# Optimization experiments

Measured on AMD Instinct MI355X. Metric: run time of the kernel, lower is better.

## Reference

```python
import jax, jax.numpy as jnp
import numpy as np

N_NODES = 50000
N_EDGES = 800000
N_RELS = 65
D = 64
N_GRAPHS = 512


def setup_inputs() -> dict:
    key = jax.random.key(0)
    ks = jax.random.split(key, 20)
    inp = {
        "node_feats": jax.random.normal(ks[0], (N_NODES, D), dtype=jnp.float32),
        "etypes": jax.random.randint(ks[1], (N_EDGES,), 0, N_RELS),
        "src": jax.random.randint(ks[2], (N_EDGES,), 0, N_NODES),
        "dst": jax.random.randint(ks[3], (N_EDGES,), 0, N_NODES),
        "graph_ids": jnp.sort(jax.random.randint(ks[4], (N_NODES,), 0, N_GRAPHS)),
    }
    s = 1.0 / np.sqrt(D)
    # 3 RGCN layers: per-relation weights (basis with num_bases=num_rels == full) + bias
    for i, k in zip(range(1, 4), (ks[5], ks[6], ks[7])):
        inp[f"W_rel{i}"] = jax.random.normal(k, (N_RELS, D, D), dtype=jnp.float32) * s
        inp[f"b{i}"] = jnp.zeros((D,), dtype=jnp.float32)
    # 3 FC layers
    for i, k in zip(range(1, 4), (ks[8], ks[9], ks[10])):
        inp[f"fc_W{i}"] = jax.random.normal(k, (D, D), dtype=jnp.float32) * s
        inp[f"fc_b{i}"] = jnp.zeros((D,), dtype=jnp.float32)
    inp["pred_W"] = jax.random.normal(ks[11], (D, 2), dtype=jnp.float32) * s
    inp["pred_b"] = jnp.zeros((2,), dtype=jnp.float32)
    return inp


def _rgcn_layer(h, W, b, etypes, src, dst):
    # all-relation projection: [N, R, K]
    proj = jnp.einsum('nd,rdk->nrk', h, W)
    # per-edge gather of relation-specific message: [E, K]
    msg = proj[src, etypes]
    # scatter-sum into destination nodes
    agg = jax.ops.segment_sum(msg, dst, num_segments=h.shape[0])
    return jax.nn.relu(agg + b)


def reference(node_feats, etypes, src, dst, graph_ids,
              W_rel1, b1, W_rel2, b2, W_rel3, b3,
              fc_W1, fc_b1, fc_W2, fc_b2, fc_W3, fc_b3,
              pred_W, pred_b):
    h = node_feats
    h = _rgcn_layer(h, W_rel1, b1, etypes, src, dst)
    h = _rgcn_layer(h, W_rel2, b2, etypes, src, dst)
    h = _rgcn_layer(h, W_rel3, b3, etypes, src, dst)
    # sum-pool nodes per graph: [G, D]
    g = jax.ops.segment_sum(h, graph_ids, num_segments=N_GRAPHS)
    g = jax.nn.relu(g @ fc_W1 + fc_b1)
    g = jax.nn.relu(g @ fc_W2 + fc_b2)
    g = jax.nn.relu(g @ fc_W3 + fc_b3)
    return g @ pred_W + pred_b
```

## Files before the change

### kernel.cpp

```cpp
#include <hip/hip_runtime.h>
#include <hip/hip_bf16.h>

#define N_NODES 50000
#define N_EDGES 800000
#define N_RELS 65
#define DIM 64
#define N_GRAPHS 512

#define SORT_BLOCKS 256
#define CHUNK ((N_EDGES + SORT_BLOCKS - 1) / SORT_BLOCKS)

#define SCAN_BLK 512
#define NSCAN_BLKS ((N_NODES + SCAN_BLK - 1) / SCAN_BLK)

#define MSG_BLOCKS 1024
#define NWAVES (MSG_BLOCKS * 4)

typedef __attribute__((ext_vector_type(8))) short short8;
typedef __attribute__((ext_vector_type(4))) float f32x4;


__global__ void conv_h_kernel(const float* __restrict__ x, __hip_bfloat16* __restrict__ y) {
    int i = blockIdx.x * 256 + threadIdx.x;
    if (i < N_NODES * DIM) y[i] = __float2bfloat16(x[i]);
}

__global__ void conv_wt3_kernel(const float* __restrict__ W1, const float* __restrict__ W2,
                                const float* __restrict__ W3,
                                __hip_bfloat16* __restrict__ Wt1,
                                __hip_bfloat16* __restrict__ Wt2,
                                __hip_bfloat16* __restrict__ Wt3) {
    const int n = N_RELS * DIM * DIM;
    int i = blockIdx.x * 256 + threadIdx.x;
    if (i >= 3 * n) return;
    int which = i / n, j = i - which * n;
    const float* W = (which == 0) ? W1 : (which == 1) ? W2 : W3;
    __hip_bfloat16* Wt = (which == 0) ? Wt1 : (which == 1) ? Wt2 : Wt3;
    int r = j >> 12, rest = j & 4095;
    int nn = rest >> 6, k = rest & 63;
    Wt[(size_t)r * 4096 + nn * 64 + k] = __float2bfloat16(W[(size_t)r * 4096 + k * 64 + nn]);
}


__global__ __launch_bounds__(256) void hist2_kernel(const int* __restrict__ et,
                                                    int* __restrict__ blk_hist) {
    __shared__ int lh[N_RELS];
    int t = threadIdx.x, b = blockIdx.x;
    if (t < N_RELS) lh[t] = 0;
    __syncthreads();
    int lo = b * CHUNK;
    int hi = lo + CHUNK; if (hi > N_EDGES) hi = N_EDGES;
    for (int i = lo + t; i < hi; i += 256) atomicAdd(&lh[et[i]], 1);
    __syncthreads();
    if (t < N_RELS) blk_hist[b * N_RELS + t] = lh[t];
}

__global__ __launch_bounds__(256) void relwave_kernel(const int* __restrict__ blk_hist,
                                                      int* __restrict__ blk_off,
                                                      int* __restrict__ rel_tot) {
    int wave = blockIdx.x * 4 + (threadIdx.x >> 6);
    int lane = threadIdx.x & 63;
    if (wave >= N_RELS) return;
    int run = 0;
    for (int c = 0; c < SORT_BLOCKS; c += 64) {
        int b = c + lane;
        int v = blk_hist[b * N_RELS + wave];
        int x = v;
        #pragma unroll
        for (int off = 1; off < 64; off <<= 1) {
            int y = __shfl_up(x, off);
            if (lane >= off) x += y;
        }
        blk_off[b * N_RELS + wave] = run + x - v;
        run += __shfl(x, 63);
    }
    if (lane == 0) rel_tot[wave] = run;
}

__global__ __launch_bounds__(128) void relbase_kernel(const int* __restrict__ rel_tot,
                                                      int* __restrict__ rel_ptr,
                                                      int* __restrict__ tile_base) {
    __shared__ int tot[N_RELS];
    int t = threadIdx.x;
    if (t < N_RELS) tot[t] = rel_tot[t];
    __syncthreads();
    if (t == 0) {
        int s = 0, tt = 0;
        for (int q = 0; q < N_RELS; ++q) {
            rel_ptr[q] = s; s += tot[q];
            tile_base[q] = tt; tt += (tot[q] + 15) >> 4;
        }
        rel_ptr[N_RELS] = N_EDGES;
        tile_base[N_RELS] = tt;
    }
}

__global__ __launch_bounds__(256) void scatter2_kernel(
    const int* __restrict__ et, const int* __restrict__ src,
    const int* __restrict__ dst, const int* __restrict__ blk_off,
    const int* __restrict__ rel_ptr,
    int* __restrict__ src_s, int* __restrict__ dst_s) {
    __shared__ int cur[N_RELS];
    int t = threadIdx.x, b = blockIdx.x;
    if (t < N_RELS) cur[t] = blk_off[b * N_RELS + t] + rel_ptr[t];
    __syncthreads();
    int lo = b * CHUNK;
    int hi = lo + CHUNK; if (hi > N_EDGES) hi = N_EDGES;
    for (int i = lo + t; i < hi; i += 256) {
        int r = et[i];
        int p = atomicAdd(&cur[r], 1);
        src_s[p] = src[i];
        dst_s[p] = dst[i];
    }
}


__global__ void histdst_kernel(const int* __restrict__ dst, int* __restrict__ cnt_d) {
    int i = blockIdx.x * 256 + threadIdx.x;
    if (i < N_EDGES) atomicAdd(&cnt_d[dst[i]], 1);
}

__global__ __launch_bounds__(SCAN_BLK) void scanblk_kernel(const int* __restrict__ cnt,
                                                           int* __restrict__ outv,
                                                           int* __restrict__ blk_tot) {
    __shared__ int tmp[SCAN_BLK];
    int t = threadIdx.x;
    int i = blockIdx.x * SCAN_BLK + t;
    int v = (i < N_NODES) ? cnt[i] : 0;
    tmp[t] = v;
    __syncthreads();
    for (int off = 1; off < SCAN_BLK; off <<= 1) {
        int add = (t >= off) ? tmp[t - off] : 0;
        __syncthreads();
        tmp[t] += add;
        __syncthreads();
    }
    if (i < N_NODES) outv[i] = tmp[t] - v;
    if (t == SCAN_BLK - 1) blk_tot[blockIdx.x] = tmp[t];
}

__global__ void scantop_kernel(int* __restrict__ blk_tot, int* __restrict__ blk_base) {
    if (threadIdx.x == 0 && blockIdx.x == 0) {
        int run = 0;
        for (int b = 0; b < NSCAN_BLKS; ++b) { blk_base[b] = run; run += blk_tot[b]; }
    }
}

__global__ __launch_bounds__(SCAN_BLK) void scanadd_kernel(int* __restrict__ outv,
                                                           const int* __restrict__ blk_base) {
    int i = blockIdx.x * SCAN_BLK + threadIdx.x;
    if (i < N_NODES) outv[i] += blk_base[blockIdx.x];
}

__global__ void dpos_kernel(const int* __restrict__ dst_s, int* __restrict__ cursor,
                            int* __restrict__ dpos) {
    int i = blockIdx.x * 256 + threadIdx.x;
    if (i < N_EDGES) dpos[i] = atomicAdd(&cursor[dst_s[i]], 1);
}


__global__ void histgid_kernel(const int* __restrict__ gid, int* __restrict__ cnt_g) {
    int i = blockIdx.x * 256 + threadIdx.x;
    if (i < N_NODES) atomicAdd(&cnt_g[gid[i]], 1);
}

__global__ __launch_bounds__(512) void scangid_kernel(const int* __restrict__ cnt_g,
                                                      int* __restrict__ g_ptr) {
    __shared__ int tmp[512];
    int t = threadIdx.x;
    int v = (t < N_GRAPHS) ? cnt_g[t] : 0;
    tmp[t] = v;
    __syncthreads();
    for (int off = 1; off < 512; off <<= 1) {
        int add = (t >= off) ? tmp[t - off] : 0;
        __syncthreads();
        tmp[t] += add;
        __syncthreads();
    }
    if (t < N_GRAPHS) g_ptr[t] = tmp[t] - v;
}


__global__ __launch_bounds__(256) void msg_mfma_kernel(
    const __hip_bfloat16* __restrict__ hb, const __hip_bfloat16* __restrict__ Wt,
    const int* __restrict__ rel_ptr, const int* __restrict__ tile_base,
    const int* __restrict__ src_s, const int* __restrict__ dpos,
    __hip_bfloat16* __restrict__ msg) {
    __shared__ __align__(16) unsigned short stA[4][16 * 72];
    __shared__ __align__(16) float stC[4][16 * 68];

    int t = threadIdx.x;
    int w = t >> 6, lane = t & 63;
    int quad = lane >> 4, m16 = lane & 15;
    int wave = blockIdx.x * 4 + w;

    int ntiles = tile_base[N_RELS];
    int tpw = (ntiles + NWAVES - 1) / NWAVES;
    int T = wave * tpw;
    int T1 = T + tpw; if (T1 > ntiles) T1 = ntiles;
    if (T >= T1) return;

    unsigned short* sa = &stA[w][0];
    float* sc = &stC[w][0];

    int r = 0;
    while (T >= tile_base[r + 1]) ++r;

    while (T < T1) {
        int chunk_end = tile_base[r + 1]; if (chunk_end > T1) chunk_end = T1;
        int seg_end = rel_ptr[r + 1];

        const __hip_bfloat16* Wr = Wt + (size_t)r * (DIM * DIM);
        short8 bf00 = *(const short8*)(Wr + (0 * 16 + m16) * DIM + 0 * 32 + quad * 8);
        short8 bf01 = *(const short8*)(Wr + (1 * 16 + m16) * DIM + 0 * 32 + quad * 8);
        short8 bf02 = *(const short8*)(Wr + (2 * 16 + m16) * DIM + 0 * 32 + quad * 8);
        short8 bf03 = *(const short8*)(Wr + (3 * 16 + m16) * DIM + 0 * 32 + quad * 8);
        short8 bf10 = *(const short8*)(Wr + (0 * 16 + m16) * DIM + 1 * 32 + quad * 8);
        short8 bf11 = *(const short8*)(Wr + (1 * 16 + m16) * DIM + 1 * 32 + quad * 8);
        short8 bf12 = *(const short8*)(Wr + (2 * 16 + m16) * DIM + 1 * 32 + quad * 8);
        short8 bf13 = *(const short8*)(Wr + (3 * 16 + m16) * DIM + 1 * 32 + quad * 8);

        for (; T < chunk_end; ++T) {
            int e0 = rel_ptr[r] + (T - tile_base[r]) * 16;
            int rows = seg_end - e0; if (rows > 16) rows = 16;

            int sv = 0, dp = 0;
            if (lane < rows) { sv = src_s[e0 + lane]; dp = dpos[e0 + lane]; }

            #pragma unroll
            for (int half = 0; half < 2; ++half) {
                int row = (lane >> 3) + half * 8;
                int s = __shfl(sv, row);
                uint4 d; d.x = 0u; d.y = 0u; d.z = 0u; d.w = 0u;
                if (row < rows)
                    d = *(const uint4*)(hb + (size_t)s * DIM + (lane & 7) * 8);
                *(uint4*)&sa[row * 72 + (lane & 7) * 8] = d;
            }

            short8 a0 = *(const short8*)&sa[m16 * 72 + quad * 8];
            short8 a1 = *(const short8*)&sa[m16 * 72 + 32 + quad * 8];

            f32x4 c0 = {0.f, 0.f, 0.f, 0.f}, c1 = c0, c2 = c0, c3 = c0;
            c0 = __builtin_amdgcn_mfma_f32_16x16x32_bf16(a0, bf00, c0, 0, 0, 0);
            c1 = __builtin_amdgcn_mfma_f32_16x16x32_bf16(a0, bf01, c1, 0, 0, 0);
            c2 = __builtin_amdgcn_mfma_f32_16x16x32_bf16(a0, bf02, c2, 0, 0, 0);
            c3 = __builtin_amdgcn_mfma_f32_16x16x32_bf16(a0, bf03, c3, 0, 0, 0);
            c0 = __builtin_amdgcn_mfma_f32_16x16x32_bf16(a1, bf10, c0, 0, 0, 0);
            c1 = __builtin_amdgcn_mfma_f32_16x16x32_bf16(a1, bf11, c1, 0, 0, 0);
            c2 = __builtin_amdgcn_mfma_f32_16x16x32_bf16(a1, bf12, c2, 0, 0, 0);
            c3 = __builtin_amdgcn_mfma_f32_16x16x32_bf16(a1, bf13, c3, 0, 0, 0);

            #pragma unroll
            for (int reg = 0; reg < 4; ++reg) {
                int rr = (quad * 4 + reg) * 68 + m16;
                sc[rr +  0] = c0[reg];
                sc[rr + 16] = c1[reg];
                sc[rr + 32] = c2[reg];
                sc[rr + 48] = c3[reg];
            }

            int orow = lane >> 2;
            if (orow < rows) {
                int c0i = (lane & 3) * 16;
                float vs[16];
                *(f32x4*)&vs[0]  = *(const f32x4*)&sc[orow * 68 + c0i + 0];
                *(f32x4*)&vs[4]  = *(const f32x4*)&sc[orow * 68 + c0i + 4];
                *(f32x4*)&vs[8]  = *(const f32x4*)&sc[orow * 68 + c0i + 8];
                *(f32x4*)&vs[12] = *(const f32x4*)&sc[orow * 68 + c0i + 12];
                unsigned short us[16];
                #pragma unroll
                for (int i = 0; i < 16; ++i)
                    us[i] = __hip_bfloat16_raw(__float2bfloat16(vs[i])).x;
                int dprow = __shfl(dp, orow);
                __hip_bfloat16* dst = msg + (size_t)dprow * DIM + c0i;
                *(uint4*)dst = *(const uint4*)&us[0];
                *(uint4*)(dst + 8) = *(const uint4*)&us[8];
            }
        }
        ++r;
        while (T < T1 && T >= tile_base[r + 1]) ++r;
    }
}


__global__ __launch_bounds__(256) void agg_kernel(
    const __hip_bfloat16* __restrict__ msg, const int* __restrict__ row_ptr,
    const int* __restrict__ cnt_d, const float* __restrict__ b,
    __hip_bfloat16* __restrict__ hout) {
    int wave = blockIdx.x * 4 + (threadIdx.x >> 6);
    int lane = threadIdx.x & 63;
    if (wave >= N_NODES) return;
    int j0 = row_ptr[wave];
    int n  = cnt_d[wave];
    float a0 = 0.f, a1 = 0.f, a2 = 0.f, a3 = 0.f;
    int j = 0;
    for (; j + 3 < n; j += 4) {
        a0 += __bfloat162float(msg[(size_t)(j0 + j + 0) * DIM + lane]);
        a1 += __bfloat162float(msg[(size_t)(j0 + j + 1) * DIM + lane]);
        a2 += __bfloat162float(msg[(size_t)(j0 + j + 2) * DIM + lane]);
        a3 += __bfloat162float(msg[(size_t)(j0 + j + 3) * DIM + lane]);
    }
    for (; j < n; ++j)
        a0 += __bfloat162float(msg[(size_t)(j0 + j) * DIM + lane]);
    float v = ((a0 + a1) + (a2 + a3)) + b[lane];
    hout[(size_t)wave * DIM + lane] = __float2bfloat16(v > 0.f ? v : 0.f);
}


__global__ __launch_bounds__(256) void pool_seg_kernel(
    const __hip_bfloat16* __restrict__ h, const int* __restrict__ g_ptr,
    const int* __restrict__ cnt_g, float* __restrict__ g) {
    int wave = blockIdx.x * 4 + (threadIdx.x >> 6);
    int lane = threadIdx.x & 63;
    if (wave >= N_GRAPHS) return;
    int j0 = g_ptr[wave];
    int n  = cnt_g[wave];
    float a0 = 0.f, a1 = 0.f;
    int j = 0;
    for (; j + 1 < n; j += 2) {
        a0 += __bfloat162float(h[(size_t)(j0 + j) * DIM + lane]);
        a1 += __bfloat162float(h[(size_t)(j0 + j + 1) * DIM + lane]);
    }
    if (j < n) a0 += __bfloat162float(h[(size_t)(j0 + j) * DIM + lane]);
    g[(size_t)wave * DIM + lane] = a0 + a1;
}


__global__ __launch_bounds__(256) void fc_kernel(
    const float* __restrict__ g,
    const float* __restrict__ W1, const float* __restrict__ b1,
    const float* __restrict__ W2, const float* __restrict__ b2,
    const float* __restrict__ W3, const float* __restrict__ b3,
    const float* __restrict__ pW, const float* __restrict__ pb,
    float* __restrict__ out) {
    int wave = blockIdx.x * 4 + (threadIdx.x >> 6);
    int lane = threadIdx.x & 63;
    if (wave >= N_GRAPHS) return;

    float v = g[(size_t)wave * DIM + lane];

    const float* Ws[3] = {W1, W2, W3};
    const float* bs[3] = {b1, b2, b3};
    for (int l = 0; l < 3; ++l) {
        float acc = bs[l][lane];
        const float* __restrict__ Wl = Ws[l];
        #pragma unroll
        for (int d = 0; d < DIM; ++d)
            acc += __shfl(v, d) * Wl[d * DIM + lane];
        v = acc > 0.f ? acc : 0.f;
    }

    float p0 = v * pW[lane * 2 + 0];
    float p1 = v * pW[lane * 2 + 1];
    #pragma unroll
    for (int off = 32; off > 0; off >>= 1) {
        p0 += __shfl_down(p0, off);
        p1 += __shfl_down(p1, off);
    }
    if (lane == 0) {
        out[wave * 2 + 0] = p0 + pb[0];
        out[wave * 2 + 1] = p1 + pb[1];
    }
}


extern "C" void kernel_launch(void* const* d_in, const int* in_sizes, int n_in,
                              void* d_out, int out_size, void* d_ws, size_t ws_size,
                              hipStream_t stream) {
    const float* node_feats = (const float*)d_in[0];
    const int*   etypes     = (const int*)d_in[1];
    const int*   src        = (const int*)d_in[2];
    const int*   dst        = (const int*)d_in[3];
    const int*   graph_ids  = (const int*)d_in[4];
    const float* W1 = (const float*)d_in[5];
    const float* b1 = (const float*)d_in[6];
    const float* W2 = (const float*)d_in[7];
    const float* b2 = (const float*)d_in[8];
    const float* W3 = (const float*)d_in[9];
    const float* b3 = (const float*)d_in[10];
    const float* fcW1 = (const float*)d_in[11];
    const float* fcb1 = (const float*)d_in[12];
    const float* fcW2 = (const float*)d_in[13];
    const float* fcb2 = (const float*)d_in[14];
    const float* fcW3 = (const float*)d_in[15];
    const float* fcb3 = (const float*)d_in[16];
    const float* pW = (const float*)d_in[17];
    const float* pb = (const float*)d_in[18];
    float* out = (float*)d_out;

    char* p = (char*)d_ws;
    auto alloc = [&](size_t bytes) -> void* {
        void* r = (void*)p;
        p += (bytes + 255) & ~(size_t)255;
        return r;
    };
    int* blk_hist  = (int*)alloc((size_t)SORT_BLOCKS * N_RELS * sizeof(int));
    int* blk_off   = (int*)alloc((size_t)SORT_BLOCKS * N_RELS * sizeof(int));
    int* rel_tot   = (int*)alloc(N_RELS * sizeof(int));
    int* rel_ptr   = (int*)alloc((N_RELS + 1) * sizeof(int));
    int* tile_base = (int*)alloc((N_RELS + 1) * sizeof(int));
    int* src_s     = (int*)alloc((size_t)N_EDGES * sizeof(int));
    int* dst_s     = (int*)alloc((size_t)N_EDGES * sizeof(int));
    int* dpos      = (int*)alloc((size_t)N_EDGES * sizeof(int));
    int* cnt_d     = (int*)alloc((size_t)N_NODES * sizeof(int));
    int* row_ptr   = (int*)alloc((size_t)N_NODES * sizeof(int));
    int* cursor_d  = (int*)alloc((size_t)N_NODES * sizeof(int));
    int* blk_tot   = (int*)alloc(NSCAN_BLKS * sizeof(int));
    int* blk_base  = (int*)alloc(NSCAN_BLKS * sizeof(int));
    int* cnt_g     = (int*)alloc(N_GRAPHS * sizeof(int));
    int* g_ptr     = (int*)alloc(N_GRAPHS * sizeof(int));
    float* g       = (float*)alloc((size_t)N_GRAPHS * DIM * sizeof(float));
    __hip_bfloat16* hb0 = (__hip_bfloat16*)alloc((size_t)N_NODES * DIM * sizeof(__hip_bfloat16));
    __hip_bfloat16* hb1 = (__hip_bfloat16*)alloc((size_t)N_NODES * DIM * sizeof(__hip_bfloat16));
    __hip_bfloat16* Wt1 = (__hip_bfloat16*)alloc((size_t)N_RELS * DIM * DIM * sizeof(__hip_bfloat16));
    __hip_bfloat16* Wt2 = (__hip_bfloat16*)alloc((size_t)N_RELS * DIM * DIM * sizeof(__hip_bfloat16));
    __hip_bfloat16* Wt3 = (__hip_bfloat16*)alloc((size_t)N_RELS * DIM * DIM * sizeof(__hip_bfloat16));
    __hip_bfloat16* msg = (__hip_bfloat16*)alloc((size_t)N_EDGES * DIM * sizeof(__hip_bfloat16));

    const int EBLK = (N_EDGES + 255) / 256;
    const int HBLK = (N_NODES * DIM + 255) / 256;
    const int W3BLK = (3 * N_RELS * DIM * DIM + 255) / 256;
    const int NBLK256 = (N_NODES + 255) / 256;
    const int AGG_BLOCKS = (N_NODES + 3) / 4;

    conv_h_kernel<<<HBLK, 256, 0, stream>>>(node_feats, hb0);
    conv_wt3_kernel<<<W3BLK, 256, 0, stream>>>(W1, W2, W3, Wt1, Wt2, Wt3);

    hist2_kernel<<<SORT_BLOCKS, 256, 0, stream>>>(etypes, blk_hist);
    relwave_kernel<<<(N_RELS + 3) / 4, 256, 0, stream>>>(blk_hist, blk_off, rel_tot);
    relbase_kernel<<<1, 128, 0, stream>>>(rel_tot, rel_ptr, tile_base);
    scatter2_kernel<<<SORT_BLOCKS, 256, 0, stream>>>(etypes, src, dst, blk_off, rel_ptr,
                                                     src_s, dst_s);

    hipMemsetAsync(cnt_d, 0, (size_t)N_NODES * sizeof(int), stream);
    histdst_kernel<<<EBLK, 256, 0, stream>>>(dst, cnt_d);
    scanblk_kernel<<<NSCAN_BLKS, SCAN_BLK, 0, stream>>>(cnt_d, row_ptr, blk_tot);
    scantop_kernel<<<1, 64, 0, stream>>>(blk_tot, blk_base);
    scanadd_kernel<<<NSCAN_BLKS, SCAN_BLK, 0, stream>>>(row_ptr, blk_base);
    hipMemcpyAsync(cursor_d, row_ptr, (size_t)N_NODES * sizeof(int),
                   hipMemcpyDeviceToDevice, stream);
    dpos_kernel<<<EBLK, 256, 0, stream>>>(dst_s, cursor_d, dpos);

    hipMemsetAsync(cnt_g, 0, N_GRAPHS * sizeof(int), stream);
    histgid_kernel<<<NBLK256, 256, 0, stream>>>(graph_ids, cnt_g);
    scangid_kernel<<<1, 512, 0, stream>>>(cnt_g, g_ptr);

    msg_mfma_kernel<<<MSG_BLOCKS, 256, 0, stream>>>(hb0, Wt1, rel_ptr, tile_base,
                                                    src_s, dpos, msg);
    agg_kernel<<<AGG_BLOCKS, 256, 0, stream>>>(msg, row_ptr, cnt_d, b1, hb1);

    msg_mfma_kernel<<<MSG_BLOCKS, 256, 0, stream>>>(hb1, Wt2, rel_ptr, tile_base,
                                                    src_s, dpos, msg);
    agg_kernel<<<AGG_BLOCKS, 256, 0, stream>>>(msg, row_ptr, cnt_d, b2, hb0);

    msg_mfma_kernel<<<MSG_BLOCKS, 256, 0, stream>>>(hb0, Wt3, rel_ptr, tile_base,
                                                    src_s, dpos, msg);
    agg_kernel<<<AGG_BLOCKS, 256, 0, stream>>>(msg, row_ptr, cnt_d, b3, hb1);

    pool_seg_kernel<<<(N_GRAPHS + 3) / 4, 256, 0, stream>>>(hb1, g_ptr, cnt_g, g);
    fc_kernel<<<(N_GRAPHS + 3) / 4, 256, 0, stream>>>(g, fcW1, fcb1, fcW2, fcb2,
                                                      fcW3, fcb3, pW, pb, out);
}
```

Baseline: 452.0 us.

## Prefetch gathers in message kernel, vectorize aggregation, fuse pool+FC and memsets

The message MFMA kernel now software-pipelines its work: it prefetches the next tile's source rows and the index loads two tiles ahead, which is meant to hide gather latency. The aggregation and pooling kernels switch to 16-byte bf16 loads across 8 row groups, followed by a shuffle reduction. Pooling is fused with the FC layers, and the memsets and the cursor memcpy are folded into existing kernels to cut launch count. The trade-off is higher register pressure, and padded tail rows are now loaded with clamped indices instead of zeroed.

```diff
diff --git a/kernel.cpp b/kernel.cpp
--- a/kernel.cpp
+++ b/kernel.cpp
@@ -20,9 +20,12 @@
 typedef __attribute__((ext_vector_type(4))) float f32x4;
 
 
-__global__ void conv_h_kernel(const float* __restrict__ x, __hip_bfloat16* __restrict__ y) {
+__global__ void conv_h_zero_kernel(const float* __restrict__ x, __hip_bfloat16* __restrict__ y,
+                                   int* __restrict__ cnt_d, int* __restrict__ cnt_g) {
     int i = blockIdx.x * 256 + threadIdx.x;
     if (i < N_NODES * DIM) y[i] = __float2bfloat16(x[i]);
+    if (i < N_NODES) cnt_d[i] = 0;
+    if (i < N_GRAPHS) cnt_g[i] = 0;
 }
 
 __global__ void conv_wt3_kernel(const float* __restrict__ W1, const float* __restrict__ W2,
@@ -147,9 +150,14 @@
 }
 
 __global__ __launch_bounds__(SCAN_BLK) void scanadd_kernel(int* __restrict__ outv,
+                                                           int* __restrict__ cursor,
                                                            const int* __restrict__ blk_base) {
     int i = blockIdx.x * SCAN_BLK + threadIdx.x;
-    if (i < N_NODES) outv[i] += blk_base[blockIdx.x];
+    if (i < N_NODES) {
+        int v = outv[i] + blk_base[blockIdx.x];
+        outv[i] = v;
+        cursor[i] = v;
+    }
 }
 
 __global__ void dpos_kernel(const int* __restrict__ dst_s, int* __restrict__ cursor,
@@ -208,6 +216,7 @@
 
     while (T < T1) {
         int chunk_end = tile_base[r + 1]; if (chunk_end > T1) chunk_end = T1;
+        int e_base = rel_ptr[r], t_base = tile_base[r];
         int seg_end = rel_ptr[r + 1];
 
         const __hip_bfloat16* Wr = Wt + (size_t)r * (DIM * DIM);
@@ -220,21 +229,46 @@
         short8 bf12 = *(const short8*)(Wr + (2 * 16 + m16) * DIM + 1 * 32 + quad * 8);
         short8 bf13 = *(const short8*)(Wr + (3 * 16 + m16) * DIM + 1 * 32 + quad * 8);
 
+        auto eidx = [&](int TT) {
+            int i = e_base + (TT - t_base) * 16 + lane;
+            return i < N_EDGES ? i : N_EDGES - 1;
+        };
+
+        int sv_c, dp_c, sv_n = 0, dp_n = 0, sv_nn = 0, dp_nn = 0;
+        uint4 g0_c, g1_c;
+        {
+            int i0 = eidx(T);
+            sv_c = src_s[i0]; dp_c = dpos[i0];
+            int r0 = lane >> 3;
+            int s0 = __shfl(sv_c, r0);
+            int s1 = __shfl(sv_c, r0 + 8);
+            g0_c = *(const uint4*)(hb + (size_t)s0 * DIM + (lane & 7) * 8);
+            g1_c = *(const uint4*)(hb + (size_t)s1 * DIM + (lane & 7) * 8);
+            if (T + 1 < chunk_end) {
+                int i1 = eidx(T + 1);
+                sv_n = src_s[i1]; dp_n = dpos[i1];
+            }
+        }
+
         for (; T < chunk_end; ++T) {
-            int e0 = rel_ptr[r] + (T - tile_base[r]) * 16;
+            int e0 = e_base + (T - t_base) * 16;
             int rows = seg_end - e0; if (rows > 16) rows = 16;
 
-            int sv = 0, dp = 0;
-            if (lane < rows) { sv = src_s[e0 + lane]; dp = dpos[e0 + lane]; }
-
-            #pragma unroll
-            for (int half = 0; half < 2; ++half) {
-                int row = (lane >> 3) + half * 8;
-                int s = __shfl(sv, row);
-                uint4 d; d.x = 0u; d.y = 0u; d.z = 0u; d.w = 0u;
-                if (row < rows)
-                    d = *(const uint4*)(hb + (size_t)s * DIM + (lane & 7) * 8);
-                *(uint4*)&sa[row * 72 + (lane & 7) * 8] = d;
+            int r0 = lane >> 3;
+            *(uint4*)&sa[r0 * 72 + (lane & 7) * 8] = g0_c;
+            *(uint4*)&sa[(r0 + 8) * 72 + (lane & 7) * 8] = g1_c;
+
+            uint4 g0_n, g1_n;
+            bool hasN = (T + 1 < chunk_end);
+            if (hasN) {
+                int s0 = __shfl(sv_n, r0);
+                int s1 = __shfl(sv_n, r0 + 8);
+                g0_n = *(const uint4*)(hb + (size_t)s0 * DIM + (lane & 7) * 8);
+                g1_n = *(const uint4*)(hb + (size_t)s1 * DIM + (lane & 7) * 8);
+            }
+            if (T + 2 < chunk_end) {
+                int i2 = eidx(T + 2);
+                sv_nn = src_s[i2]; dp_nn = dpos[i2];
             }
 
             short8 a0 = *(const short8*)&sa[m16 * 72 + quad * 8];
@@ -271,11 +305,15 @@
                 #pragma unroll
                 for (int i = 0; i < 16; ++i)
                     us[i] = __hip_bfloat16_raw(__float2bfloat16(vs[i])).x;
-                int dprow = __shfl(dp, orow);
+                int dprow = __shfl(dp_c, orow);
                 __hip_bfloat16* dst = msg + (size_t)dprow * DIM + c0i;
                 *(uint4*)dst = *(const uint4*)&us[0];
                 *(uint4*)(dst + 8) = *(const uint4*)&us[8];
             }
+
+            if (hasN) { g0_c = g0_n; g1_c = g1_n; }
+            sv_c = sv_n; dp_c = dp_n;
+            sv_n = sv_nn; dp_n = dp_nn;
         }
         ++r;
         while (T < T1 && T >= tile_base[r + 1]) ++r;
@@ -292,42 +330,44 @@
     if (wave >= N_NODES) return;
     int j0 = row_ptr[wave];
     int n  = cnt_d[wave];
-    float a0 = 0.f, a1 = 0.f, a2 = 0.f, a3 = 0.f;
-    int j = 0;
-    for (; j + 3 < n; j += 4) {
-        a0 += __bfloat162float(msg[(size_t)(j0 + j + 0) * DIM + lane]);
-        a1 += __bfloat162float(msg[(size_t)(j0 + j + 1) * DIM + lane]);
-        a2 += __bfloat162float(msg[(size_t)(j0 + j + 2) * DIM + lane]);
-        a3 += __bfloat162float(msg[(size_t)(j0 + j + 3) * DIM + lane]);
-    }
-    for (; j < n; ++j)
-        a0 += __bfloat162float(msg[(size_t)(j0 + j) * DIM + lane]);
-    float v = ((a0 + a1) + (a2 + a3)) + b[lane];
-    hout[(size_t)wave * DIM + lane] = __float2bfloat16(v > 0.f ? v : 0.f);
-}
-
-
-__global__ __launch_bounds__(256) void pool_seg_kernel(
+    int rgrp = lane >> 3, dgrp = lane & 7;
+
+    float a[8] = {0.f, 0.f, 0.f, 0.f, 0.f, 0.f, 0.f, 0.f};
+    for (int jj = 0; jj < n; jj += 8) {
+        int row = jj + rgrp;
+        if (row < n) {
+            uint4 d = *(const uint4*)(msg + (size_t)(j0 + row) * DIM + dgrp * 8);
+            a[0] += __uint_as_float(d.x << 16);
+            a[1] += __uint_as_float(d.x & 0xffff0000u);
+            a[2] += __uint_as_float(d.y << 16);
+            a[3] += __uint_as_float(d.y & 0xffff0000u);
+            a[4] += __uint_as_float(d.z << 16);
+            a[5] += __uint_as_float(d.z & 0xffff0000u);
+            a[6] += __uint_as_float(d.w << 16);
+            a[7] += __uint_as_float(d.w & 0xffff0000u);
+        }
+    }
+    #pragma unroll
+    for (int i = 0; i < 8; ++i) {
+        a[i] += __shfl_xor(a[i], 8);
+        a[i] += __shfl_xor(a[i], 16);
+        a[i] += __shfl_xor(a[i], 32);
+    }
+    if (rgrp == 0) {
+        unsigned short us[8];
+        #pragma unroll
+        for (int i = 0; i < 8; ++i) {
+            float v = a[i] + b[dgrp * 8 + i];
+            us[i] = __hip_bfloat16_raw(__float2bfloat16(v > 0.f ? v : 0.f)).x;
+        }
+        *(uint4*)(hout + (size_t)wave * DIM + dgrp * 8) = *(const uint4*)us;
+    }
+}
+
+
+__global__ __launch_bounds__(256) void poolfc_kernel(
     const __hip_bfloat16* __restrict__ h, const int* __restrict__ g_ptr,
-    const int* __restrict__ cnt_g, float* __restrict__ g) {
-    int wave = blockIdx.x * 4 + (threadIdx.x >> 6);
-    int lane = threadIdx.x & 63;
-    if (wave >= N_GRAPHS) return;
-    int j0 = g_ptr[wave];
-    int n  = cnt_g[wave];
-    float a0 = 0.f, a1 = 0.f;
-    int j = 0;
-    for (; j + 1 < n; j += 2) {
-        a0 += __bfloat162float(h[(size_t)(j0 + j) * DIM + lane]);
-        a1 += __bfloat162float(h[(size_t)(j0 + j + 1) * DIM + lane]);
-    }
-    if (j < n) a0 += __bfloat162float(h[(size_t)(j0 + j) * DIM + lane]);
-    g[(size_t)wave * DIM + lane] = a0 + a1;
-}
-
-
-__global__ __launch_bounds__(256) void fc_kernel(
-    const float* __restrict__ g,
+    const int* __restrict__ cnt_g,
     const float* __restrict__ W1, const float* __restrict__ b1,
     const float* __restrict__ W2, const float* __restrict__ b2,
     const float* __restrict__ W3, const float* __restrict__ b3,
@@ -336,20 +376,55 @@
     int wave = blockIdx.x * 4 + (threadIdx.x >> 6);
     int lane = threadIdx.x & 63;
     if (wave >= N_GRAPHS) return;
-
-    float v = g[(size_t)wave * DIM + lane];
-
-    const float* Ws[3] = {W1, W2, W3};
-    const float* bs[3] = {b1, b2, b3};
-    for (int l = 0; l < 3; ++l) {
-        float acc = bs[l][lane];
-        const float* __restrict__ Wl = Ws[l];
+    int j0 = g_ptr[wave];
+    int n  = cnt_g[wave];
+    int rgrp = lane >> 3, dgrp = lane & 7;
+
+    float a[8] = {0.f, 0.f, 0.f, 0.f, 0.f, 0.f, 0.f, 0.f};
+    for (int jj = 0; jj < n; jj += 8) {
+        int row = jj + rgrp;
+        if (row < n) {
+            uint4 d = *(const uint4*)(h + (size_t)(j0 + row) * DIM + dgrp * 8);
+            a[0] += __uint_as_float(d.x << 16);
+            a[1] += __uint_as_float(d.x & 0xffff0000u);
+            a[2] += __uint_as_float(d.y << 16);
+            a[3] += __uint_as_float(d.y & 0xffff0000u);
+            a[4] += __uint_as_float(d.z << 16);
+            a[5] += __uint_as_float(d.z & 0xffff0000u);
+            a[6] += __uint_as_float(d.w << 16);
+            a[7] += __uint_as_float(d.w & 0xffff0000u);
+        }
+    }
+    #pragma unroll
+    for (int i = 0; i < 8; ++i) {
+        a[i] += __shfl_xor(a[i], 8);
+        a[i] += __shfl_xor(a[i], 16);
+        a[i] += __shfl_xor(a[i], 32);
+    }
+    float v;
+    {
+        float acc = b1[lane];
+        #pragma unroll
+        for (int o = 0; o < 8; ++o)
+            #pragma unroll
+            for (int q = 0; q < 8; ++q)
+                acc += __shfl(a[o], q) * W1[(q * 8 + o) * DIM + lane];
+        v = acc > 0.f ? acc : 0.f;
+    }
+    {
+        float acc = b2[lane];
         #pragma unroll
         for (int d = 0; d < DIM; ++d)
-            acc += __shfl(v, d) * Wl[d * DIM + lane];
+            acc += __shfl(v, d) * W2[d * DIM + lane];
         v = acc > 0.f ? acc : 0.f;
     }
-
+    {
+        float acc = b3[lane];
+        #pragma unroll
+        for (int d = 0; d < DIM; ++d)
+            acc += __shfl(v, d) * W3[d * DIM + lane];
+        v = acc > 0.f ? acc : 0.f;
+    }
     float p0 = v * pW[lane * 2 + 0];
     float p1 = v * pW[lane * 2 + 1];
     #pragma unroll
@@ -409,7 +484,6 @@
     int* blk_base  = (int*)alloc(NSCAN_BLKS * sizeof(int));
     int* cnt_g     = (int*)alloc(N_GRAPHS * sizeof(int));
     int* g_ptr     = (int*)alloc(N_GRAPHS * sizeof(int));
-    float* g       = (float*)alloc((size_t)N_GRAPHS * DIM * sizeof(float));
     __hip_bfloat16* hb0 = (__hip_bfloat16*)alloc((size_t)N_NODES * DIM * sizeof(__hip_bfloat16));
     __hip_bfloat16* hb1 = (__hip_bfloat16*)alloc((size_t)N_NODES * DIM * sizeof(__hip_bfloat16));
     __hip_bfloat16* Wt1 = (__hip_bfloat16*)alloc((size_t)N_RELS * DIM * DIM * sizeof(__hip_bfloat16));
@@ -423,7 +497,7 @@
     const int NBLK256 = (N_NODES + 255) / 256;
     const int AGG_BLOCKS = (N_NODES + 3) / 4;
 
-    conv_h_kernel<<<HBLK, 256, 0, stream>>>(node_feats, hb0);
+    conv_h_zero_kernel<<<HBLK, 256, 0, stream>>>(node_feats, hb0, cnt_d, cnt_g);
     conv_wt3_kernel<<<W3BLK, 256, 0, stream>>>(W1, W2, W3, Wt1, Wt2, Wt3);
 
     hist2_kernel<<<SORT_BLOCKS, 256, 0, stream>>>(etypes, blk_hist);
@@ -432,16 +506,12 @@
     scatter2_kernel<<<SORT_BLOCKS, 256, 0, stream>>>(etypes, src, dst, blk_off, rel_ptr,
                                                      src_s, dst_s);
 
-    hipMemsetAsync(cnt_d, 0, (size_t)N_NODES * sizeof(int), stream);
     histdst_kernel<<<EBLK, 256, 0, stream>>>(dst, cnt_d);
     scanblk_kernel<<<NSCAN_BLKS, SCAN_BLK, 0, stream>>>(cnt_d, row_ptr, blk_tot);
     scantop_kernel<<<1, 64, 0, stream>>>(blk_tot, blk_base);
-    scanadd_kernel<<<NSCAN_BLKS, SCAN_BLK, 0, stream>>>(row_ptr, blk_base);
-    hipMemcpyAsync(cursor_d, row_ptr, (size_t)N_NODES * sizeof(int),
-                   hipMemcpyDeviceToDevice, stream);
+    scanadd_kernel<<<NSCAN_BLKS, SCAN_BLK, 0, stream>>>(row_ptr, cursor_d, blk_base);
     dpos_kernel<<<EBLK, 256, 0, stream>>>(dst_s, cursor_d, dpos);
 
-    hipMemsetAsync(cnt_g, 0, N_GRAPHS * sizeof(int), stream);
     histgid_kernel<<<NBLK256, 256, 0, stream>>>(graph_ids, cnt_g);
     scangid_kernel<<<1, 512, 0, stream>>>(cnt_g, g_ptr);
 
@@ -457,7 +527,7 @@
                                                     src_s, dpos, msg);
     agg_kernel<<<AGG_BLOCKS, 256, 0, stream>>>(msg, row_ptr, cnt_d, b3, hb1);
 
-    pool_seg_kernel<<<(N_GRAPHS + 3) / 4, 256, 0, stream>>>(hb1, g_ptr, cnt_g, g);
-    fc_kernel<<<(N_GRAPHS + 3) / 4, 256, 0, stream>>>(g, fcW1, fcb1, fcW2, fcb2,
-                                                      fcW3, fcb3, pW, pb, out);
-}
+    poolfc_kernel<<<(N_GRAPHS + 3) / 4, 256, 0, stream>>>(hb1, g_ptr, cnt_g,
+                                                          fcW1, fcb1, fcW2, fcb2,
+                                                          fcW3, fcb3, pW, pb, out);
+}
```

New measurement: 421.4 us. -6.8%, faster.
